# Optimization experiments

Measured on AMD Instinct MI355X. Metric: run time of the kernel, lower is better.

Reference implementation:

```python
import jax, jax.numpy as jnp
import numpy as np


def dct_matrix(N, dtype=jnp.float32):
    # DCT-II orthonormal basis: D[k, n] = s_k * cos(pi * (n + 0.5) * k / N)
    n = jnp.arange(N, dtype=dtype)
    k = jnp.arange(N, dtype=dtype)
    M = jnp.cos(jnp.pi * (n[None, :] + 0.5) * k[:, None] / N)
    scale = jnp.full((N,), jnp.sqrt(2.0 / N), dtype=dtype).at[0].set(jnp.sqrt(1.0 / N))
    return scale[:, None] * M  # [K, N]


def setup_inputs() -> dict:
    key = jax.random.key(0)
    k1, k2, k3, k4 = jax.random.split(key, 4)
    B, C, H, W = 64, 3, 512, 512
    x = jax.random.normal(k1, (B, C, H, W), dtype=jnp.float32)
    attention = jax.random.uniform(k2, (H, W), dtype=jnp.float32)
    row_weights = jax.random.uniform(k3, (H,), dtype=jnp.float32)
    col_weights = jax.random.uniform(k4, (W,), dtype=jnp.float32)
    return {"x": x, "attention": attention, "row_weights": row_weights,
            "col_weights": col_weights}


def reference(x, attention, row_weights, col_weights):
    B, C, H, W = x.shape
    Dw = dct_matrix(W, x.dtype)  # DCT along last axis
    Dh = dct_matrix(H, x.dtype)  # DCT along second-to-last axis
    # dct(x, axis=-1): contract columns; dct(., axis=-2): contract rows
    x_dct = jnp.einsum('kh,bchw,lw->bckl', Dh, x, Dw)
    gray = x_dct.mean(axis=1)                 # [B, H, W]
    weighted = gray * attention               # [B, H, W]
    row_sum = weighted.mean(axis=2)           # [B, H]
    col_sum = weighted.mean(axis=1)           # [B, W]
    row_output = (row_sum * row_weights).mean(axis=1)  # [B]
    col_output = (col_sum * col_weights).mean(axis=1)  # [B]
    return jax.nn.sigmoid(jnp.stack([col_output, row_output], axis=1))  # [B, 2]
```

## Files before the change

### kernel.cpp

```cpp
#include <hip/hip_runtime.h>
#include <hip/hip_bf16.h>
#include <math.h>


typedef __attribute__((ext_vector_type(8))) short bf16x8;
typedef __attribute__((ext_vector_type(4))) float f32x4;

#define NFULL 512
#define HWTOT 262144
#define SCALE_M (1.0f / 786432.0f)
#define KC_BLOCKS 2048

static __device__ __forceinline__ unsigned short f_to_bf16(float f) {
  union { float f; unsigned int i; } v; v.f = f;
  unsigned int r = v.i + 0x7FFFu + ((v.i >> 16) & 1u);
  return (unsigned short)(r >> 16);
}

__global__ void k0_prep(const float* __restrict__ att,
                        const float* __restrict__ rw,
                        const float* __restrict__ cw,
                        unsigned short* __restrict__ DT,
                        unsigned short* __restrict__ Arw,
                        unsigned short* __restrict__ Acw) {
  int idx = blockIdx.x * blockDim.x + threadIdx.x;
  int r = idx >> 9;
  int c = idx & 511;
  unsigned int ph = ((unsigned int)(2 * r + 1) * (unsigned int)c) & 2047u;
  float s = (c == 0) ? 0.04419417382415922f
                     : 0.0625f;
  DT[idx] = f_to_bf16(s * cospif((float)ph * (1.0f / 1024.0f)));
  float a = att[idx];
  Arw[idx] = f_to_bf16(a * rw[r]);
  Acw[idx] = f_to_bf16(a * cw[c]);
}

__global__ void ka_gemm(const unsigned short* __restrict__ DT,
                        const unsigned short* __restrict__ Arw,
                        const unsigned short* __restrict__ Acw,
                        unsigned short* __restrict__ T1T,
                        unsigned short* __restrict__ T2T) {
  int wave = (blockIdx.x * blockDim.x + threadIdx.x) >> 6;
  int lane = threadIdx.x & 63;
  int tk = wave >> 5, tw = wave & 31;
  int row_a = tk * 16 + (lane & 15);
  int row_b = tw * 16 + (lane & 15);
  int koff = (lane >> 4) * 8;

  const bf16x8* A1 = (const bf16x8*)(Arw + row_a * NFULL);
  const bf16x8* A2 = (const bf16x8*)(Acw + row_a * NFULL);
  const bf16x8* Bp = (const bf16x8*)(DT  + row_b * NFULL);

  f32x4 acc1 = {0.f, 0.f, 0.f, 0.f};
  f32x4 acc2 = {0.f, 0.f, 0.f, 0.f};
#pragma unroll 4
  for (int l0 = 0; l0 < NFULL; l0 += 32) {
    int e = (l0 + koff) >> 3;
    bf16x8 b = Bp[e];
    acc1 = __builtin_amdgcn_mfma_f32_16x16x32_bf16(A1[e], b, acc1, 0, 0, 0);
    acc2 = __builtin_amdgcn_mfma_f32_16x16x32_bf16(A2[e], b, acc2, 0, 0, 0);
  }
  int col = lane & 15, r0 = (lane >> 4) * 4;
  int w  = tw * 16 + col;
  int k0 = tk * 16 + r0;
  unsigned int g0 = f_to_bf16(acc1[0]) | ((unsigned int)f_to_bf16(acc1[1]) << 16);
  unsigned int g1 = f_to_bf16(acc1[2]) | ((unsigned int)f_to_bf16(acc1[3]) << 16);
  unsigned int c0 = f_to_bf16(acc2[0]) | ((unsigned int)f_to_bf16(acc2[1]) << 16);
  unsigned int c1 = f_to_bf16(acc2[2]) | ((unsigned int)f_to_bf16(acc2[3]) << 16);
  *(uint2*)(T1T + w * NFULL + k0) = make_uint2(g0, g1);
  *(uint2*)(T2T + w * NFULL + k0) = make_uint2(c0, c1);
}

__global__ void kb_gemm(const unsigned short* __restrict__ DT,
                        const unsigned short* __restrict__ T1T,
                        const unsigned short* __restrict__ T2T,
                        float* __restrict__ Mrow,
                        float* __restrict__ Mcol) {
  int wave = (blockIdx.x * blockDim.x + threadIdx.x) >> 6;
  int lane = threadIdx.x & 63;
  int th = wave >> 5, tw = wave & 31;
  int row_a = th * 16 + (lane & 15);
  int row_b = tw * 16 + (lane & 15);
  int koff = (lane >> 4) * 8;

  const bf16x8* Ap = (const bf16x8*)(DT  + row_a * NFULL);
  const bf16x8* Rp = (const bf16x8*)(T1T + row_b * NFULL);
  const bf16x8* Cp = (const bf16x8*)(T2T + row_b * NFULL);

  f32x4 accR = {0.f, 0.f, 0.f, 0.f};
  f32x4 accC = {0.f, 0.f, 0.f, 0.f};
#pragma unroll 4
  for (int k0 = 0; k0 < NFULL; k0 += 32) {
    int e = (k0 + koff) >> 3;
    bf16x8 a = Ap[e];
    accR = __builtin_amdgcn_mfma_f32_16x16x32_bf16(a, Rp[e], accR, 0, 0, 0);
    accC = __builtin_amdgcn_mfma_f32_16x16x32_bf16(a, Cp[e], accC, 0, 0, 0);
  }
  int col = lane & 15, r0 = (lane >> 4) * 4;
  int h0 = th * 16 + r0;
  int w  = tw * 16 + col;
#pragma unroll
  for (int j = 0; j < 4; ++j) {
    Mrow[(h0 + j) * NFULL + w] = accR[j] * SCALE_M;
    Mcol[(h0 + j) * NFULL + w] = accC[j] * SCALE_M;
  }
}

__global__ void kc_dot(const float* __restrict__ x,
                       const float* __restrict__ Mcol,
                       const float* __restrict__ Mrow,
                       float* __restrict__ partial) {
  int b   = blockIdx.x >> 5;
  int sub = blockIdx.x & 31;
  int tid = threadIdx.x;
  const f32x4* xb = (const f32x4*)x + (size_t)b * 196608;
  const f32x4* mc = (const f32x4*)Mcol;
  const f32x4* mr = (const f32x4*)Mrow;

  float a0 = 0.f, a1 = 0.f;
  int base = sub * 2048 + tid;
#pragma unroll
  for (int it = 0; it < 8; ++it) {
    int i = base + it * 256;
    f32x4 x0 = xb[i];
    f32x4 x1 = xb[i + 65536];
    f32x4 x2 = xb[i + 131072];
    f32x4 m0 = mc[i];
    f32x4 m1 = mr[i];
    f32x4 sv = x0 + x1 + x2;
    a0 += sv.x * m0.x + sv.y * m0.y + sv.z * m0.z + sv.w * m0.w;
    a1 += sv.x * m1.x + sv.y * m1.y + sv.z * m1.z + sv.w * m1.w;
  }

  int lane = tid & 63, wv = tid >> 6;
#pragma unroll
  for (int off = 32; off > 0; off >>= 1) {
    a0 += __shfl_down(a0, off);
    a1 += __shfl_down(a1, off);
  }
  __shared__ float red[8];
  if (lane == 0) { red[wv * 2] = a0; red[wv * 2 + 1] = a1; }
  __syncthreads();
  if (tid == 0) {
    float s0 = red[0] + red[2] + red[4] + red[6];
    float s1 = red[1] + red[3] + red[5] + red[7];
    partial[(b * 32 + sub) * 2 + 0] = s0;
    partial[(b * 32 + sub) * 2 + 1] = s1;
  }
}

__global__ void kd_final(const float* __restrict__ partial, float* __restrict__ out) {
  int t = threadIdx.x;
  int b = t >> 1, o = t & 1;
  float s = 0.f;
#pragma unroll
  for (int j = 0; j < 32; ++j) s += partial[(b * 32 + j) * 2 + o];
  out[b * 2 + o] = 1.0f / (1.0f + expf(-s));
}

extern "C" void kernel_launch(void* const* d_in, const int* in_sizes, int n_in,
                              void* d_out, int out_size, void* d_ws, size_t ws_size,
                              hipStream_t stream) {
  const float* x   = (const float*)d_in[0];
  const float* att = (const float*)d_in[1];
  const float* rw  = (const float*)d_in[2];
  const float* cw  = (const float*)d_in[3];
  float* out = (float*)d_out;

  unsigned short* DT  = (unsigned short*)d_ws;
  unsigned short* Arw = DT  + HWTOT;
  unsigned short* Acw = Arw + HWTOT;
  unsigned short* T1T = Acw + HWTOT;
  unsigned short* T2T = T1T + HWTOT;
  float* Mrow    = (float*)(T2T + HWTOT);
  float* Mcol    = Mrow + HWTOT;
  float* partial = Mcol + HWTOT;

  k0_prep<<<1024, 256, 0, stream>>>(att, rw, cw, DT, Arw, Acw);
  ka_gemm<<<256, 256, 0, stream>>>(DT, Arw, Acw, T1T, T2T);
  kb_gemm<<<256, 256, 0, stream>>>(DT, T1T, T2T, Mrow, Mcol);
  kc_dot<<<KC_BLOCKS, 256, 0, stream>>>(x, Mcol, Mrow, partial);
  kd_final<<<1, 128, 0, stream>>>(partial, out);
}
```

Baseline: 57.99 us.

## Fuse prep and two GEMM stages into one cooperative kernel with grid syncs

The three small launches (prep, first GEMM, second GEMM) become a single cooperative kernel of 256 blocks that separates the phases with grid.sync(). The goal is to remove two launch gaps and tail effects on these tiny stages. The dot kernel also gets manual register double-buffering, issuing the next iteration's loads before the current FMA work. The cost is that the prep phase now runs on 256 blocks instead of 1024, and grid-wide barriers have their own overhead.

New measurement: 120.2 us. +107.2%, slower.

```diff
diff --git a/kernel.cpp b/kernel.cpp
--- a/kernel.cpp
+++ b/kernel.cpp
@@ -1,6 +1,9 @@
 #include <hip/hip_runtime.h>
 #include <hip/hip_bf16.h>
+#include <hip/hip_cooperative_groups.h>
 #include <math.h>
+
+namespace cg = cooperative_groups;
 
 
 typedef __attribute__((ext_vector_type(8))) short bf16x8;
@@ -17,119 +20,129 @@
   return (unsigned short)(r >> 16);
 }
 
-__global__ void k0_prep(const float* __restrict__ att,
-                        const float* __restrict__ rw,
-                        const float* __restrict__ cw,
-                        unsigned short* __restrict__ DT,
-                        unsigned short* __restrict__ Arw,
-                        unsigned short* __restrict__ Acw) {
-  int idx = blockIdx.x * blockDim.x + threadIdx.x;
-  int r = idx >> 9;
-  int c = idx & 511;
-  unsigned int ph = ((unsigned int)(2 * r + 1) * (unsigned int)c) & 2047u;
-  float s = (c == 0) ? 0.04419417382415922f
-                     : 0.0625f;
-  DT[idx] = f_to_bf16(s * cospif((float)ph * (1.0f / 1024.0f)));
-  float a = att[idx];
-  Arw[idx] = f_to_bf16(a * rw[r]);
-  Acw[idx] = f_to_bf16(a * cw[c]);
-}
+__global__ __launch_bounds__(256, 1) void kprep(
+    const float* __restrict__ att, const float* __restrict__ rw,
+    const float* __restrict__ cw,
+    unsigned short* __restrict__ DT, unsigned short* __restrict__ Arw,
+    unsigned short* __restrict__ Acw,
+    unsigned short* __restrict__ T1T, unsigned short* __restrict__ T2T,
+    float* __restrict__ Mrow, float* __restrict__ Mcol) {
+  cg::grid_group grid = cg::this_grid();
+  int gtid = blockIdx.x * 256 + threadIdx.x;
 
-__global__ void ka_gemm(const unsigned short* __restrict__ DT,
-                        const unsigned short* __restrict__ Arw,
-                        const unsigned short* __restrict__ Acw,
-                        unsigned short* __restrict__ T1T,
-                        unsigned short* __restrict__ T2T) {
-  int wave = (blockIdx.x * blockDim.x + threadIdx.x) >> 6;
-  int lane = threadIdx.x & 63;
-  int tk = wave >> 5, tw = wave & 31;
-  int row_a = tk * 16 + (lane & 15);
-  int row_b = tw * 16 + (lane & 15);
-  int koff = (lane >> 4) * 8;
-
-  const bf16x8* A1 = (const bf16x8*)(Arw + row_a * NFULL);
-  const bf16x8* A2 = (const bf16x8*)(Acw + row_a * NFULL);
-  const bf16x8* Bp = (const bf16x8*)(DT  + row_b * NFULL);
-
-  f32x4 acc1 = {0.f, 0.f, 0.f, 0.f};
-  f32x4 acc2 = {0.f, 0.f, 0.f, 0.f};
-#pragma unroll 4
-  for (int l0 = 0; l0 < NFULL; l0 += 32) {
-    int e = (l0 + koff) >> 3;
-    bf16x8 b = Bp[e];
-    acc1 = __builtin_amdgcn_mfma_f32_16x16x32_bf16(A1[e], b, acc1, 0, 0, 0);
-    acc2 = __builtin_amdgcn_mfma_f32_16x16x32_bf16(A2[e], b, acc2, 0, 0, 0);
-  }
-  int col = lane & 15, r0 = (lane >> 4) * 4;
-  int w  = tw * 16 + col;
-  int k0 = tk * 16 + r0;
-  unsigned int g0 = f_to_bf16(acc1[0]) | ((unsigned int)f_to_bf16(acc1[1]) << 16);
-  unsigned int g1 = f_to_bf16(acc1[2]) | ((unsigned int)f_to_bf16(acc1[3]) << 16);
-  unsigned int c0 = f_to_bf16(acc2[0]) | ((unsigned int)f_to_bf16(acc2[1]) << 16);
-  unsigned int c1 = f_to_bf16(acc2[2]) | ((unsigned int)f_to_bf16(acc2[3]) << 16);
-  *(uint2*)(T1T + w * NFULL + k0) = make_uint2(g0, g1);
-  *(uint2*)(T2T + w * NFULL + k0) = make_uint2(c0, c1);
-}
-
-__global__ void kb_gemm(const unsigned short* __restrict__ DT,
-                        const unsigned short* __restrict__ T1T,
-                        const unsigned short* __restrict__ T2T,
-                        float* __restrict__ Mrow,
-                        float* __restrict__ Mcol) {
-  int wave = (blockIdx.x * blockDim.x + threadIdx.x) >> 6;
-  int lane = threadIdx.x & 63;
-  int th = wave >> 5, tw = wave & 31;
-  int row_a = th * 16 + (lane & 15);
-  int row_b = tw * 16 + (lane & 15);
-  int koff = (lane >> 4) * 8;
-
-  const bf16x8* Ap = (const bf16x8*)(DT  + row_a * NFULL);
-  const bf16x8* Rp = (const bf16x8*)(T1T + row_b * NFULL);
-  const bf16x8* Cp = (const bf16x8*)(T2T + row_b * NFULL);
-
-  f32x4 accR = {0.f, 0.f, 0.f, 0.f};
-  f32x4 accC = {0.f, 0.f, 0.f, 0.f};
-#pragma unroll 4
-  for (int k0 = 0; k0 < NFULL; k0 += 32) {
-    int e = (k0 + koff) >> 3;
-    bf16x8 a = Ap[e];
-    accR = __builtin_amdgcn_mfma_f32_16x16x32_bf16(a, Rp[e], accR, 0, 0, 0);
-    accC = __builtin_amdgcn_mfma_f32_16x16x32_bf16(a, Cp[e], accC, 0, 0, 0);
-  }
-  int col = lane & 15, r0 = (lane >> 4) * 4;
-  int h0 = th * 16 + r0;
-  int w  = tw * 16 + col;
 #pragma unroll
   for (int j = 0; j < 4; ++j) {
-    Mrow[(h0 + j) * NFULL + w] = accR[j] * SCALE_M;
-    Mcol[(h0 + j) * NFULL + w] = accC[j] * SCALE_M;
+    int idx = gtid + j * 65536;
+    int r = idx >> 9;
+    int c = idx & 511;
+    unsigned int ph = ((unsigned int)(2 * r + 1) * (unsigned int)c) & 2047u;
+    float s = (c == 0) ? 0.04419417382415922f : 0.0625f;
+    DT[idx] = f_to_bf16(s * cospif((float)ph * (1.0f / 1024.0f)));
+    float a = att[idx];
+    Arw[idx] = f_to_bf16(a * rw[r]);
+    Acw[idx] = f_to_bf16(a * cw[c]);
+  }
+  grid.sync();
+
+  {
+    int wave = (blockIdx.x << 2) + (threadIdx.x >> 6);
+    int lane = threadIdx.x & 63;
+    int tk = wave >> 5, tw = wave & 31;
+    int row_a = tk * 16 + (lane & 15);
+    int row_b = tw * 16 + (lane & 15);
+    int koff = (lane >> 4) * 8;
+
+    const bf16x8* A1 = (const bf16x8*)(Arw + row_a * NFULL);
+    const bf16x8* A2 = (const bf16x8*)(Acw + row_a * NFULL);
+    const bf16x8* Bp = (const bf16x8*)(DT  + row_b * NFULL);
+
+    f32x4 acc1 = {0.f, 0.f, 0.f, 0.f};
+    f32x4 acc2 = {0.f, 0.f, 0.f, 0.f};
+#pragma unroll 4
+    for (int l0 = 0; l0 < NFULL; l0 += 32) {
+      int e = (l0 + koff) >> 3;
+      bf16x8 b = Bp[e];
+      acc1 = __builtin_amdgcn_mfma_f32_16x16x32_bf16(A1[e], b, acc1, 0, 0, 0);
+      acc2 = __builtin_amdgcn_mfma_f32_16x16x32_bf16(A2[e], b, acc2, 0, 0, 0);
+    }
+    int col = lane & 15, r0 = (lane >> 4) * 4;
+    int w  = tw * 16 + col;
+    int k0 = tk * 16 + r0;
+    unsigned int g0 = f_to_bf16(acc1[0]) | ((unsigned int)f_to_bf16(acc1[1]) << 16);
+    unsigned int g1 = f_to_bf16(acc1[2]) | ((unsigned int)f_to_bf16(acc1[3]) << 16);
+    unsigned int c0 = f_to_bf16(acc2[0]) | ((unsigned int)f_to_bf16(acc2[1]) << 16);
+    unsigned int c1 = f_to_bf16(acc2[2]) | ((unsigned int)f_to_bf16(acc2[3]) << 16);
+    *(uint2*)(T1T + w * NFULL + k0) = make_uint2(g0, g1);
+    *(uint2*)(T2T + w * NFULL + k0) = make_uint2(c0, c1);
+  }
+  grid.sync();
+
+  {
+    int wave = (blockIdx.x << 2) + (threadIdx.x >> 6);
+    int lane = threadIdx.x & 63;
+    int th = wave >> 5, tw = wave & 31;
+    int row_a = th * 16 + (lane & 15);
+    int row_b = tw * 16 + (lane & 15);
+    int koff = (lane >> 4) * 8;
+
+    const bf16x8* Ap = (const bf16x8*)(DT  + row_a * NFULL);
+    const bf16x8* Rp = (const bf16x8*)(T1T + row_b * NFULL);
+    const bf16x8* Cp = (const bf16x8*)(T2T + row_b * NFULL);
+
+    f32x4 accR = {0.f, 0.f, 0.f, 0.f};
+    f32x4 accC = {0.f, 0.f, 0.f, 0.f};
+#pragma unroll 4
+    for (int k0 = 0; k0 < NFULL; k0 += 32) {
+      int e = (k0 + koff) >> 3;
+      bf16x8 a = Ap[e];
+      accR = __builtin_amdgcn_mfma_f32_16x16x32_bf16(a, Rp[e], accR, 0, 0, 0);
+      accC = __builtin_amdgcn_mfma_f32_16x16x32_bf16(a, Cp[e], accC, 0, 0, 0);
+    }
+    int col = lane & 15, r0 = (lane >> 4) * 4;
+    int h0 = th * 16 + r0;
+    int w  = tw * 16 + col;
+#pragma unroll
+    for (int j = 0; j < 4; ++j) {
+      Mrow[(h0 + j) * NFULL + w] = accR[j] * SCALE_M;
+      Mcol[(h0 + j) * NFULL + w] = accC[j] * SCALE_M;
+    }
   }
 }
 
-__global__ void kc_dot(const float* __restrict__ x,
-                       const float* __restrict__ Mcol,
-                       const float* __restrict__ Mrow,
-                       float* __restrict__ partial) {
+__global__ __launch_bounds__(256) void kc_dot(const float* __restrict__ x,
+                                              const float* __restrict__ Mcol,
+                                              const float* __restrict__ Mrow,
+                                              float* __restrict__ partial) {
   int b   = blockIdx.x >> 5;
   int sub = blockIdx.x & 31;
   int tid = threadIdx.x;
-  const f32x4* xb = (const f32x4*)x + (size_t)b * 196608;
-  const f32x4* mc = (const f32x4*)Mcol;
-  const f32x4* mr = (const f32x4*)Mrow;
+  const f32x4* __restrict__ xb = (const f32x4*)x + (size_t)b * 196608;
+  const f32x4* __restrict__ mc = (const f32x4*)Mcol;
+  const f32x4* __restrict__ mr = (const f32x4*)Mrow;
+
+  int base = sub * 2048 + tid;
+
+  f32x4 m0 = mc[base];
+  f32x4 m1 = mr[base];
+  f32x4 x0 = xb[base];
+  f32x4 x1 = xb[base + 65536];
+  f32x4 x2 = xb[base + 131072];
 
   float a0 = 0.f, a1 = 0.f;
-  int base = sub * 2048 + tid;
 #pragma unroll
   for (int it = 0; it < 8; ++it) {
-    int i = base + it * 256;
-    f32x4 x0 = xb[i];
-    f32x4 x1 = xb[i + 65536];
-    f32x4 x2 = xb[i + 131072];
-    f32x4 m0 = mc[i];
-    f32x4 m1 = mr[i];
-    f32x4 sv = x0 + x1 + x2;
-    a0 += sv.x * m0.x + sv.y * m0.y + sv.z * m0.z + sv.w * m0.w;
-    a1 += sv.x * m1.x + sv.y * m1.y + sv.z * m1.z + sv.w * m1.w;
+    f32x4 cm0 = m0, cm1 = m1, cx0 = x0, cx1 = x1, cx2 = x2;
+    if (it < 7) {
+      int i = base + (it + 1) * 256;
+      m0 = mc[i];
+      m1 = mr[i];
+      x0 = xb[i];
+      x1 = xb[i + 65536];
+      x2 = xb[i + 131072];
+    }
+    f32x4 sv = cx0 + cx1 + cx2;
+    a0 += sv.x * cm0.x + sv.y * cm0.y + sv.z * cm0.z + sv.w * cm0.w;
+    a1 += sv.x * cm1.x + sv.y * cm1.y + sv.z * cm1.z + sv.w * cm1.w;
   }
 
   int lane = tid & 63, wv = tid >> 6;
@@ -176,9 +189,9 @@
   float* Mcol    = Mrow + HWTOT;
   float* partial = Mcol + HWTOT;
 
-  k0_prep<<<1024, 256, 0, stream>>>(att, rw, cw, DT, Arw, Acw);
-  ka_gemm<<<256, 256, 0, stream>>>(DT, Arw, Acw, T1T, T2T);
-  kb_gemm<<<256, 256, 0, stream>>>(DT, T1T, T2T, Mrow, Mcol);
+  void* args[] = {(void*)&att, (void*)&rw, (void*)&cw, (void*)&DT, (void*)&Arw,
+                  (void*)&Acw, (void*)&T1T, (void*)&T2T, (void*)&Mrow, (void*)&Mcol};
+  hipLaunchCooperativeKernel((void*)kprep, dim3(256), dim3(256), args, 0, stream);
   kc_dot<<<KC_BLOCKS, 256, 0, stream>>>(x, Mcol, Mrow, partial);
   kd_final<<<1, 128, 0, stream>>>(partial, out);
 }
```
